# Kernel tuning notes

Measured on AMD Instinct MI355X. Metric: run time of the kernel, lower is better.

The kernel has to match this reference:

```python
import jax, jax.numpy as jnp
import numpy as np

H, HD, D = 16, 64, 1024
SCALE = HD ** -0.5
TEMP = 1.0
EPS = 1e-5

def setup_inputs() -> dict:
    key = jax.random.key(0)
    ks = jax.random.split(key, 10)
    B, N = 2, 2048
    lim = 1.0 / np.sqrt(D)
    def lin(k, out_d, in_d):
        k1, k2 = jax.random.split(k)
        W = jax.random.uniform(k1, (out_d, in_d), jnp.float32, -lim, lim)
        b = jax.random.uniform(k2, (out_d,), jnp.float32, -lim, lim)
        return W, b
    Wq, bq = lin(ks[0], H * HD, D)
    Wk, bk = lin(ks[1], H * HD, D)
    Wv, bv = lin(ks[2], H * HD, D)
    Wo, bo = lin(ks[3], D, H * HD)
    return {
        "x": jax.random.normal(ks[4], (B, N, D), jnp.float32),
        "adaptive_scale": jnp.ones((H,), jnp.float32),
        "Wq": Wq, "bq": bq, "Wk": Wk, "bk": bk, "Wv": Wv, "bv": bv,
        "Wo": Wo, "bo": bo,
        "gamma": jnp.ones((D,), jnp.float32),
        "beta": jnp.zeros((D,), jnp.float32),
    }

def reference(x, adaptive_scale, Wq, bq, Wk, bk, Wv, bv, Wo, bo, gamma, beta):
    B, N, _ = x.shape
    # self-attention: context = x
    Q = (x @ Wq.T + bq).reshape(B, N, H, HD)
    K = (x @ Wk.T + bk).reshape(B, N, H, HD)
    V = (x @ Wv.T + bv).reshape(B, N, H, HD)
    # per-head adaptive scale folded into scores (matches naive QK^T * scale / temp)
    scores = jnp.einsum('bnhd,bmhd->bhnm', Q, K)
    scores = scores * (SCALE * adaptive_scale)[None, :, None, None] / TEMP
    w = jax.nn.softmax(scores, axis=-1)  # [B,H,N,N]
    attn = jnp.einsum('bhnm,bmhd->bnhd', w, V).reshape(B, N, H * HD)
    y = x + (attn @ Wo.T + bo)
    mu = jnp.mean(y, axis=-1, keepdims=True)
    var = jnp.var(y, axis=-1, keepdims=True)
    return (y - mu) / jnp.sqrt(var + EPS) * gamma + beta
```

## Files before the change

kernel.cpp:

```cpp
#include <hip/hip_runtime.h>
#include <hip/hip_bf16.h>

using bf16 = __hip_bfloat16;
typedef __attribute__((ext_vector_type(8))) short short8;
typedef __attribute__((ext_vector_type(4))) short short4v;
typedef __attribute__((ext_vector_type(4))) float f32x4;

#define MFMA16(a, b, c) __builtin_amdgcn_mfma_f32_16x16x32_bf16((a), (b), (c), 0, 0, 0)

__device__ inline void async16(bf16* lds, const bf16* g) {
  __builtin_amdgcn_global_load_lds(
      (const __attribute__((address_space(1))) void*)g,
      (__attribute__((address_space(3))) void*)lds, 16, 0, 0);
}

__device__ inline short bfs(float x) {
  union { bf16 h; short s; } u; u.h = __float2bfloat16(x); return u.s;
}
__device__ inline short4v pack4(float a, float b, float c, float d) {
  short4v r; r[0] = bfs(a); r[1] = bfs(b); r[2] = bfs(c); r[3] = bfs(d); return r;
}
__device__ inline short4v pack4t(float a, float b, float c, float d) {
  unsigned lo = __builtin_amdgcn_perm(__float_as_uint(b), __float_as_uint(a), 0x07060302u);
  unsigned hi = __builtin_amdgcn_perm(__float_as_uint(d), __float_as_uint(c), 0x07060302u);
  union { unsigned u[2]; short4v v; } r;
  r.u[0] = lo; r.u[1] = hi;
  return r.v;
}

__global__ __launch_bounds__(256) void cvt_all(
    const float* __restrict__ x,  const float* __restrict__ Wq,
    const float* __restrict__ Wk, const float* __restrict__ Wv,
    const float* __restrict__ Wo,
    bf16* __restrict__ xb, bf16* __restrict__ Wqb, bf16* __restrict__ Wkb,
    bf16* __restrict__ Wvb, bf16* __restrict__ Wob) {
  int i = blockIdx.x * 256 + threadIdx.x;
  const float* s; bf16* d; int off;
  if (i < 1048576)      { s = x;  d = xb;  off = i; }
  else if (i < 1310720) { s = Wq; d = Wqb; off = i - 1048576; }
  else if (i < 1572864) { s = Wk; d = Wkb; off = i - 1310720; }
  else if (i < 1835008) { s = Wv; d = Wvb; off = i - 1572864; }
  else                  { s = Wo; d = Wob; off = i - 1835008; }
  float4 v = ((const float4*)s)[off];
  short4v o = pack4(v.x, v.y, v.z, v.w);
  *(short4v*)&d[(size_t)off * 4] = o;
}

__global__ __launch_bounds__(256) void gemm_qkv(
    const bf16* __restrict__ A,
    const bf16* __restrict__ Wq, const bf16* __restrict__ Wk, const bf16* __restrict__ Wv,
    const float* __restrict__ bq, const float* __restrict__ bk, const float* __restrict__ bv,
    const float* __restrict__ asc,
    bf16* __restrict__ Qb, bf16* __restrict__ Kb, bf16* __restrict__ Vtb) {
  __shared__ __align__(16) bf16 As[128 * 32];
  __shared__ __align__(16) bf16 Bs[128 * 32];
  __shared__ __align__(16) bf16 scrT[4][16 * 68];

  const int tid = threadIdx.x;
  const int lane = tid & 63;
  const int w = tid >> 6;
  const int m0 = blockIdx.x * 128;
  const int region = blockIdx.y >> 3;
  const int n0loc = (blockIdx.y & 7) * 128;
  const int wm = (w >> 1) * 64;
  const int wn = (w & 1) * 64;
  const int rq = lane & 15;
  const int quad = lane >> 4;
  const int kq = quad * 8;

  const bf16* W = region == 0 ? Wq : (region == 1 ? Wk : Wv);
  const float* bias = region == 0 ? bq : (region == 1 ? bk : bv);
  bf16* C = region == 0 ? Qb : (region == 1 ? Kb : Vtb);

  f32x4 acc[4][4] = {};
  const bf16* Ag = A + (size_t)m0 * 1024;
  const bf16* Wg = W + (size_t)n0loc * 1024;

  for (int k0 = 0; k0 < 1024; k0 += 32) {
    __syncthreads();
#pragma unroll
    for (int rep = 0; rep < 2; ++rep) {
      int c = tid + rep * 256;
      int row = c >> 2;
      int ce = (c & 3) * 8;
      async16(&As[c * 8], Ag + (size_t)row * 1024 + k0 + ce);
      async16(&Bs[c * 8], Wg + (size_t)row * 1024 + k0 + ce);
    }
    __syncthreads();

    short8 a[4], b[4];
#pragma unroll
    for (int i = 0; i < 4; ++i) a[i] = *(const short8*)&As[(wm + i * 16 + rq) * 32 + kq];
#pragma unroll
    for (int j = 0; j < 4; ++j) b[j] = *(const short8*)&Bs[(wn + j * 16 + rq) * 32 + kq];
#pragma unroll
    for (int i = 0; i < 4; ++i)
#pragma unroll
      for (int j = 0; j < 4; ++j) acc[i][j] = MFMA16(a[i], b[j], acc[i][j]);
  }

  const float LOG2E = 1.44269504088896f;
  if (region < 2) {
#pragma unroll
    for (int i = 0; i < 4; ++i)
#pragma unroll
      for (int j = 0; j < 4; ++j)
#pragma unroll
        for (int r2 = 0; r2 < 4; ++r2) {
          int m = m0 + wm + i * 16 + quad * 4 + r2;
          int nr = n0loc + wn + j * 16 + rq;
          int bb = m >> 11, t = m & 2047, h = nr >> 6, hd = nr & 63;
          float v = acc[i][j][r2] + bias[nr];
          if (region == 0) v *= 0.125f * asc[h] * LOG2E;
          C[(((size_t)(bb * 16 + h)) * 2048 + t) * 64 + hd] = __float2bfloat16(v);
        }
  } else {
    const int bb = m0 >> 11;
    const int h = (n0loc + wn) >> 6;
    const int tbase = (m0 & 2047) + wm;
    bf16* scr = scrT[w];
#pragma unroll
    for (int j = 0; j < 4; ++j) {
      int nr = n0loc + wn + j * 16 + rq;
      float bi = bias[nr];
#pragma unroll
      for (int i = 0; i < 4; ++i) {
        short4v pv = pack4(acc[i][j][0] + bi, acc[i][j][1] + bi,
                           acc[i][j][2] + bi, acc[i][j][3] + bi);
        *(short4v*)&scr[rq * 68 + i * 16 + quad * 4] = pv;
      }
#pragma unroll
      for (int pp = 0; pp < 4; ++pp) {
        int hdl = pp * 4 + quad;
        short4v v4 = *(const short4v*)&scr[hdl * 68 + rq * 4];
        size_t addr = (((size_t)(bb * 16 + h)) * 64 + j * 16 + hdl) * 2048 + tbase + rq * 4;
        *(short4v*)&C[addr] = v4;
      }
    }
  }
}

__global__ __launch_bounds__(256) void gemm_out(
    const bf16* __restrict__ A, const bf16* __restrict__ W,
    const float* __restrict__ bias, const float* __restrict__ R,
    float* __restrict__ Y) {
  __shared__ __align__(16) bf16 As[128 * 32];
  __shared__ __align__(16) bf16 Bs[128 * 32];

  const int tid = threadIdx.x;
  const int lane = tid & 63;
  const int w = tid >> 6;
  const int m0 = blockIdx.x * 128;
  const int n0 = blockIdx.y * 128;
  const int wm = (w >> 1) * 64;
  const int wn = (w & 1) * 64;
  const int rq = lane & 15;
  const int quad = lane >> 4;
  const int kq = quad * 8;

  f32x4 acc[4][4] = {};
  const bf16* Ag = A + (size_t)m0 * 1024;
  const bf16* Wg = W + (size_t)n0 * 1024;

  for (int k0 = 0; k0 < 1024; k0 += 32) {
    __syncthreads();
#pragma unroll
    for (int rep = 0; rep < 2; ++rep) {
      int c = tid + rep * 256;
      int row = c >> 2;
      int ce = (c & 3) * 8;
      async16(&As[c * 8], Ag + (size_t)row * 1024 + k0 + ce);
      async16(&Bs[c * 8], Wg + (size_t)row * 1024 + k0 + ce);
    }
    __syncthreads();

    short8 a[4], b[4];
#pragma unroll
    for (int i = 0; i < 4; ++i) a[i] = *(const short8*)&As[(wm + i * 16 + rq) * 32 + kq];
#pragma unroll
    for (int j = 0; j < 4; ++j) b[j] = *(const short8*)&Bs[(wn + j * 16 + rq) * 32 + kq];
#pragma unroll
    for (int i = 0; i < 4; ++i)
#pragma unroll
      for (int j = 0; j < 4; ++j) acc[i][j] = MFMA16(a[i], b[j], acc[i][j]);
  }

#pragma unroll
  for (int i = 0; i < 4; ++i)
#pragma unroll
    for (int j = 0; j < 4; ++j)
#pragma unroll
      for (int r2 = 0; r2 < 4; ++r2) {
        int m = m0 + wm + i * 16 + quad * 4 + r2;
        int n = n0 + wn + j * 16 + rq;
        Y[(size_t)m * 1024 + n] = acc[i][j][r2] + bias[n] + R[(size_t)m * 1024 + n];
      }
}

#define LP 72
__global__ __launch_bounds__(256, 2) void attn_kernel(
    const bf16* __restrict__ Qb, const bf16* __restrict__ Kb,
    const bf16* __restrict__ Vtb,
    bf16* __restrict__ P0, bf16* __restrict__ P1, float* __restrict__ lbuf) {
  __shared__ __align__(16) bf16 Ks[64 * 64];
  __shared__ __align__(16) bf16 Vs[64 * 64];
  __shared__ __align__(16) bf16 Ps[4][64 * LP];

  const int q0 = blockIdx.x * 256;
  const int h = blockIdx.y;
  const int b = blockIdx.z & 1;
  const int half = blockIdx.z >> 1;
  const int tid = threadIdx.x;
  const int lane = tid & 63;
  const int w = tid >> 6;
  const int rq = lane & 15;
  const int quad = lane >> 4;
  const int kq = quad * 8;

  const size_t head = ((size_t)(b * 16 + h)) * 2048 * 64;
  const bf16* Qh = Qb + head;
  const bf16* Kh = Kb + head;
  const bf16* Vh = Vtb + head;

  short8 aq[4][2];
#pragma unroll
  for (int s = 0; s < 4; ++s) {
    const bf16* qrow = Qh + (size_t)(q0 + w * 64 + s * 16 + rq) * 64;
    aq[s][0] = *(const short8*)&qrow[kq];
    aq[s][1] = *(const short8*)&qrow[kq + 32];
  }

  short8 ones;
#pragma unroll
  for (int i = 0; i < 8; ++i) ones[i] = (short)0x3F80;

  const int srow = lane >> 3;
  const int rowK = (tid & 7) * 0;
  (void)rowK;
  const int swsV = ((lane & 7) ^ srow) * 8;
  const int c0 = (quad ^ (rq & 7)) * 8;
  const int c1 = c0 ^ 32;

  f32x4 accO[4][4] = {};
  f32x4 lacc[4] = {};

  const int kt0 = half * 16;
  for (int kt = kt0; kt < kt0 + 16; ++kt) {
    __syncthreads();
#pragma unroll
    for (int t = 0; t < 2; ++t) {
      int rb = w * 16 + t * 8;
      int row = rb + srow;
      int swsK = ((lane & 7) ^ ((row >> 2) & 7)) * 8;
      async16(&Ks[rb * 64 + lane * 8], Kh + (size_t)(kt * 64 + row) * 64 + swsK);
      async16(&Vs[rb * 64 + lane * 8], Vh + (size_t)row * 2048 + kt * 64 + swsV);
    }
    __syncthreads();

    short8 bk[4][2];
#pragma unroll
    for (int j = 0; j < 4; ++j) {
      const bf16* kr = &Ks[(rq * 4 + j) * 64];
      bk[j][0] = *(const short8*)&kr[c0];
      bk[j][1] = *(const short8*)&kr[c1];
    }

#pragma unroll
    for (int s = 0; s < 4; ++s) {
      f32x4 S[4] = {};
#pragma unroll
      for (int j = 0; j < 4; ++j) {
        S[j] = MFMA16(aq[s][0], bk[j][0], S[j]);
        S[j] = MFMA16(aq[s][1], bk[j][1], S[j]);
      }
#pragma unroll
      for (int r = 0; r < 4; ++r) {
        short4v pv = pack4t(exp2f(S[0][r]), exp2f(S[1][r]),
                            exp2f(S[2][r]), exp2f(S[3][r]));
        *(short4v*)&Ps[w][(s * 16 + quad * 4 + r) * LP + rq * 4] = pv;
      }
    }

    short8 bv[4][2];
#pragma unroll
    for (int dt = 0; dt < 4; ++dt) {
      const bf16* vr = &Vs[(dt * 16 + rq) * 64];
      bv[dt][0] = *(const short8*)&vr[c0];
      bv[dt][1] = *(const short8*)&vr[c1];
    }
#pragma unroll
    for (int s = 0; s < 4; ++s) {
      short8 ap0 = *(const short8*)&Ps[w][(s * 16 + rq) * LP + kq];
      short8 ap1 = *(const short8*)&Ps[w][(s * 16 + rq) * LP + kq + 32];
#pragma unroll
      for (int dt = 0; dt < 4; ++dt) {
        accO[s][dt] = MFMA16(ap0, bv[dt][0], accO[s][dt]);
        accO[s][dt] = MFMA16(ap1, bv[dt][1], accO[s][dt]);
      }
      lacc[s] = MFMA16(ap0, ones, lacc[s]);
      lacc[s] = MFMA16(ap1, ones, lacc[s]);
    }
  }

  bf16* Pout = half ? P1 : P0;
  float* lout = lbuf + half * 65536;
#pragma unroll
  for (int s = 0; s < 4; ++s) {
#pragma unroll
    for (int dt = 0; dt < 4; ++dt)
#pragma unroll
      for (int r = 0; r < 4; ++r) {
        int t = q0 + w * 64 + s * 16 + quad * 4 + r;
        int d = dt * 16 + rq;
        Pout[((size_t)(b * 2048 + t)) * 1024 + h * 64 + d] =
            __float2bfloat16(accO[s][dt][r]);
      }
    if (rq == 0) {
#pragma unroll
      for (int r = 0; r < 4; ++r) {
        int t = q0 + w * 64 + s * 16 + quad * 4 + r;
        lout[(b * 16 + h) * 2048 + t] = lacc[s][r];
      }
    }
  }
}

__global__ __launch_bounds__(256) void combine_kernel(
    bf16* __restrict__ P0, const bf16* __restrict__ P1,
    const float* __restrict__ lbuf) {
  const int row = blockIdx.x;
  const int tid = threadIdx.x;
  const int col = tid * 4;
  const int b = row >> 11, t = row & 2047;
  const int h = col >> 6;
  const float l = lbuf[(b * 16 + h) * 2048 + t] + lbuf[65536 + (b * 16 + h) * 2048 + t];
  const float rl = 1.f / l;
  size_t base = (size_t)row * 1024 + col;
  short4v p0 = *(const short4v*)&P0[base];
  short4v p1 = *(const short4v*)&P1[base];
  union { short s; bf16 h; } u;
  float v[4];
#pragma unroll
  for (int i = 0; i < 4; ++i) {
    u.s = p0[i]; float a = __bfloat162float(u.h);
    u.s = p1[i]; float c = __bfloat162float(u.h);
    v[i] = (a + c) * rl;
  }
  *(short4v*)&P0[base] = pack4(v[0], v[1], v[2], v[3]);
}

__global__ __launch_bounds__(256) void ln_kernel(
    const float* __restrict__ Y, const float* __restrict__ gamma,
    const float* __restrict__ beta, float* __restrict__ out) {
  const int row = blockIdx.x;
  const int tid = threadIdx.x;
  const int lane = tid & 63;
  const int w = tid >> 6;
  const float* y = Y + (size_t)row * 1024;

  float4 v = *(const float4*)&y[tid * 4];
  float s = v.x + v.y + v.z + v.w;
  float ss = v.x * v.x + v.y * v.y + v.z * v.z + v.w * v.w;
#pragma unroll
  for (int msk = 1; msk < 64; msk <<= 1) {
    s += __shfl_xor(s, msk);
    ss += __shfl_xor(ss, msk);
  }
  __shared__ float red[2][4];
  if (lane == 0) { red[0][w] = s; red[1][w] = ss; }
  __syncthreads();
  s = red[0][0] + red[0][1] + red[0][2] + red[0][3];
  ss = red[1][0] + red[1][1] + red[1][2] + red[1][3];
  float mean = s * (1.f / 1024.f);
  float var = ss * (1.f / 1024.f) - mean * mean;
  float rstd = rsqrtf(var + 1e-5f);
  float4 g = *(const float4*)&gamma[tid * 4];
  float4 bt = *(const float4*)&beta[tid * 4];
  float4 o;
  o.x = (v.x - mean) * rstd * g.x + bt.x;
  o.y = (v.y - mean) * rstd * g.y + bt.y;
  o.z = (v.z - mean) * rstd * g.z + bt.z;
  o.w = (v.w - mean) * rstd * g.w + bt.w;
  *(float4*)&out[(size_t)row * 1024 + tid * 4] = o;
}

extern "C" void kernel_launch(void* const* d_in, const int* in_sizes, int n_in,
                              void* d_out, int out_size, void* d_ws, size_t ws_size,
                              hipStream_t stream) {
  const float* x     = (const float*)d_in[0];
  const float* asc   = (const float*)d_in[1];
  const float* Wq    = (const float*)d_in[2];
  const float* bq    = (const float*)d_in[3];
  const float* Wk    = (const float*)d_in[4];
  const float* bk    = (const float*)d_in[5];
  const float* Wv    = (const float*)d_in[6];
  const float* bv    = (const float*)d_in[7];
  const float* Wo    = (const float*)d_in[8];
  const float* bo    = (const float*)d_in[9];
  const float* gamma = (const float*)d_in[10];
  const float* beta  = (const float*)d_in[11];
  float* out = (float*)d_out;

  char* ws = (char*)d_ws;
  const size_t MB = 1024 * 1024;
  bf16* Qb   = (bf16*)(ws);
  bf16* Kb   = (bf16*)(ws + 8 * MB);
  bf16* Vtb  = (bf16*)(ws + 16 * MB);
  bf16* attn = (bf16*)(ws + 24 * MB);
  bf16* xb   = (bf16*)(ws + 32 * MB);
  bf16* Wqb  = (bf16*)(ws + 40 * MB);
  bf16* Wkb  = (bf16*)(ws + 42 * MB);
  bf16* Wvb  = (bf16*)(ws + 44 * MB);
  bf16* Wob  = (bf16*)(ws + 46 * MB);
  float* y   = (float*)(ws);
  bf16* P1   = xb;
  float* lbuf = (float*)Wqb;

  dim3 bb(256);

  cvt_all<<<dim3(8192), bb, 0, stream>>>(x, Wq, Wk, Wv, Wo, xb, Wqb, Wkb, Wvb, Wob);
  gemm_qkv<<<dim3(32, 24), bb, 0, stream>>>(xb, Wqb, Wkb, Wvb, bq, bk, bv, asc, Qb, Kb, Vtb);
  attn_kernel<<<dim3(8, 16, 4), bb, 0, stream>>>(Qb, Kb, Vtb, attn, P1, lbuf);
  combine_kernel<<<dim3(4096), bb, 0, stream>>>(attn, P1, lbuf);
  gemm_out<<<dim3(32, 8), bb, 0, stream>>>(attn, Wob, bo, x, y);
  ln_kernel<<<dim3(4096), bb, 0, stream>>>(y, gamma, beta, out);
}
```

Before: 227.9 us.

## Stage Q/K epilogue through LDS and interleave attention QK/PV per sub-tile

The QKV GEMM epilogue for Q and K now writes tiles into per-wave LDS scratch and then emits 16-byte row stores, replacing scattered 2-byte global stores. In the attention kernel, score computation, exp and the PV MFMAs are interleaved per 16-row sub-tile using a double-buffered small P scratch, which cuts LDS footprint from 4x64 rows to 4x2x16 rows per block. This aims to improve global store coalescing and reduce LDS use, possibly raising occupancy, at the cost of tighter dependencies between QK and PV within each sub-tile.

```diff
diff --git a/kernel.cpp b/kernel.cpp
--- a/kernel.cpp
+++ b/kernel.cpp
@@ -54,7 +54,7 @@
     bf16* __restrict__ Qb, bf16* __restrict__ Kb, bf16* __restrict__ Vtb) {
   __shared__ __align__(16) bf16 As[128 * 32];
   __shared__ __align__(16) bf16 Bs[128 * 32];
-  __shared__ __align__(16) bf16 scrT[4][16 * 68];
+  __shared__ __align__(16) bf16 scrT[4][16 * 72];
 
   const int tid = threadIdx.x;
   const int lane = tid & 63;
@@ -100,25 +100,35 @@
   }
 
   const float LOG2E = 1.44269504088896f;
+  bf16* scr = scrT[w];
   if (region < 2) {
-#pragma unroll
-    for (int i = 0; i < 4; ++i)
-#pragma unroll
-      for (int j = 0; j < 4; ++j)
-#pragma unroll
-        for (int r2 = 0; r2 < 4; ++r2) {
-          int m = m0 + wm + i * 16 + quad * 4 + r2;
-          int nr = n0loc + wn + j * 16 + rq;
-          int bb = m >> 11, t = m & 2047, h = nr >> 6, hd = nr & 63;
-          float v = acc[i][j][r2] + bias[nr];
-          if (region == 0) v *= 0.125f * asc[h] * LOG2E;
-          C[(((size_t)(bb * 16 + h)) * 2048 + t) * 64 + hd] = __float2bfloat16(v);
-        }
+    const int hbase = n0loc + wn;
+    const int h = hbase >> 6;
+    const float sc = (region == 0) ? 0.125f * asc[h] * LOG2E : 1.0f;
+    const int bb = m0 >> 11;
+#pragma unroll
+    for (int i = 0; i < 4; ++i) {
+#pragma unroll
+      for (int j = 0; j < 4; ++j) {
+        float bi = bias[hbase + j * 16 + rq];
+#pragma unroll
+        for (int r = 0; r < 4; ++r)
+          scr[(quad * 4 + r) * 72 + j * 16 + rq] =
+              __float2bfloat16((acc[i][j][r] + bi) * sc);
+      }
+#pragma unroll
+      for (int p = 0; p < 2; ++p) {
+        int row = p * 8 + (lane >> 3);
+        int ch = (lane & 7) * 8;
+        short8 vv = *(const short8*)&scr[row * 72 + ch];
+        int tg = (m0 & 2047) + wm + i * 16 + row;
+        *(short8*)&C[(((size_t)(bb * 16 + h)) * 2048 + tg) * 64 + ch] = vv;
+      }
+    }
   } else {
     const int bb = m0 >> 11;
     const int h = (n0loc + wn) >> 6;
     const int tbase = (m0 & 2047) + wm;
-    bf16* scr = scrT[w];
 #pragma unroll
     for (int j = 0; j < 4; ++j) {
       int nr = n0loc + wn + j * 16 + rq;
@@ -127,12 +137,12 @@
       for (int i = 0; i < 4; ++i) {
         short4v pv = pack4(acc[i][j][0] + bi, acc[i][j][1] + bi,
                            acc[i][j][2] + bi, acc[i][j][3] + bi);
-        *(short4v*)&scr[rq * 68 + i * 16 + quad * 4] = pv;
+        *(short4v*)&scr[rq * 72 + i * 16 + quad * 4] = pv;
       }
 #pragma unroll
       for (int pp = 0; pp < 4; ++pp) {
         int hdl = pp * 4 + quad;
-        short4v v4 = *(const short4v*)&scr[hdl * 68 + rq * 4];
+        short4v v4 = *(const short4v*)&scr[hdl * 72 + rq * 4];
         size_t addr = (((size_t)(bb * 16 + h)) * 64 + j * 16 + hdl) * 2048 + tbase + rq * 4;
         *(short4v*)&C[addr] = v4;
       }
@@ -197,14 +207,13 @@
       }
 }
 
-#define LP 72
 __global__ __launch_bounds__(256, 2) void attn_kernel(
     const bf16* __restrict__ Qb, const bf16* __restrict__ Kb,
     const bf16* __restrict__ Vtb,
     bf16* __restrict__ P0, bf16* __restrict__ P1, float* __restrict__ lbuf) {
   __shared__ __align__(16) bf16 Ks[64 * 64];
   __shared__ __align__(16) bf16 Vs[64 * 64];
-  __shared__ __align__(16) bf16 Ps[4][64 * LP];
+  __shared__ __align__(16) bf16 Ps[4][2][16 * 72];
 
   const int q0 = blockIdx.x * 256;
   const int h = blockIdx.y;
@@ -235,8 +244,6 @@
   for (int i = 0; i < 8; ++i) ones[i] = (short)0x3F80;
 
   const int srow = lane >> 3;
-  const int rowK = (tid & 7) * 0;
-  (void)rowK;
   const int swsV = ((lane & 7) ^ srow) * 8;
   const int c0 = (quad ^ (rq & 7)) * 8;
   const int c1 = c0 ^ 32;
@@ -264,23 +271,6 @@
       bk[j][0] = *(const short8*)&kr[c0];
       bk[j][1] = *(const short8*)&kr[c1];
     }
-
-#pragma unroll
-    for (int s = 0; s < 4; ++s) {
-      f32x4 S[4] = {};
-#pragma unroll
-      for (int j = 0; j < 4; ++j) {
-        S[j] = MFMA16(aq[s][0], bk[j][0], S[j]);
-        S[j] = MFMA16(aq[s][1], bk[j][1], S[j]);
-      }
-#pragma unroll
-      for (int r = 0; r < 4; ++r) {
-        short4v pv = pack4t(exp2f(S[0][r]), exp2f(S[1][r]),
-                            exp2f(S[2][r]), exp2f(S[3][r]));
-        *(short4v*)&Ps[w][(s * 16 + quad * 4 + r) * LP + rq * 4] = pv;
-      }
-    }
-
     short8 bv[4][2];
 #pragma unroll
     for (int dt = 0; dt < 4; ++dt) {
@@ -288,10 +278,24 @@
       bv[dt][0] = *(const short8*)&vr[c0];
       bv[dt][1] = *(const short8*)&vr[c1];
     }
+
 #pragma unroll
     for (int s = 0; s < 4; ++s) {
-      short8 ap0 = *(const short8*)&Ps[w][(s * 16 + rq) * LP + kq];
-      short8 ap1 = *(const short8*)&Ps[w][(s * 16 + rq) * LP + kq + 32];
+      bf16* Psw = Ps[w][s & 1];
+      f32x4 S[4] = {};
+#pragma unroll
+      for (int j = 0; j < 4; ++j) {
+        S[j] = MFMA16(aq[s][0], bk[j][0], S[j]);
+        S[j] = MFMA16(aq[s][1], bk[j][1], S[j]);
+      }
+#pragma unroll
+      for (int r = 0; r < 4; ++r) {
+        short4v pv = pack4t(exp2f(S[0][r]), exp2f(S[1][r]),
+                            exp2f(S[2][r]), exp2f(S[3][r]));
+        *(short4v*)&Psw[(quad * 4 + r) * 72 + rq * 4] = pv;
+      }
+      short8 ap0 = *(const short8*)&Psw[rq * 72 + kq];
+      short8 ap1 = *(const short8*)&Psw[rq * 72 + kq + 32];
 #pragma unroll
       for (int dt = 0; dt < 4; ++dt) {
         accO[s][dt] = MFMA16(ap0, bv[dt][0], accO[s][dt]);
```

Measured after the change: 231.3 us. Within noise of the previous version (+1.5%).
